# Optimization experiments

Hardware: AMD Instinct MI355X
Metric: run time of the kernel (lower is better)

The kernel has to match this reference:

```python
import jax, jax.numpy as jnp
import numpy as np

K, N, M = 65536, 4096, 64  # observations, basis centers, features


def setup_inputs() -> dict:
    key = jax.random.key(0)
    k1, k2, k3, k4 = jax.random.split(key, 4)
    x = jax.random.normal(k1, (K, M), dtype=jnp.float32)
    x_basis = jax.random.normal(k2, (N, M), dtype=jnp.float32)
    w = jax.random.normal(k3, (1, N), dtype=jnp.float32) / np.sqrt(N)
    b = jax.random.normal(k4, (1,), dtype=jnp.float32)
    return {"x": x, "x_basis": x_basis, "w": w, "b": b}


def reference(x, x_basis, w, b):
    # pairwise squared distances ||x_i - c_j||^2, [K, N]
    x2 = jnp.sum(x * x, axis=1, keepdims=True)          # [K, 1]
    c2 = jnp.sum(x_basis * x_basis, axis=1)             # [N]
    sq = x2 + c2[None, :] - 2.0 * (x @ x_basis.T)       # [K, N]
    phi = jnp.exp(-sq)                                  # gaussian RBF
    return jax.nn.sigmoid(phi @ w.T + b)                # [K, 1]
```

## Files before the change

kernel.cpp:

```cpp
#include <hip/hip_runtime.h>


#define KOBS 65536
#define NCENT 4096
#define MFEAT 64
#define BR 64
#define BN 128
#define NCHUNK (NCENT / BN)
#define KBLK (KOBS / BR)

#define SCALE_A 2.8853900817779268f
#define QS      1.4426950408889634f
#define TSKIP   -60.0f

typedef __attribute__((ext_vector_type(4)))  float float4v;
typedef __attribute__((ext_vector_type(2)))  float float2v;
typedef __attribute__((ext_vector_type(16))) float float16v;
typedef __attribute__((ext_vector_type(8)))  int   int8v;

#if __has_builtin(__builtin_amdgcn_exp2f)
#define EXP2F(x) __builtin_amdgcn_exp2f(x)
#else
#define EXP2F(x) exp2f(x)
#endif

__global__ __launch_bounds__(256) void rbf_prep(
    const float* __restrict__ xb, const float* __restrict__ w,
    char* __restrict__ cb, float2v* __restrict__ hc2w) {
    const int bid = blockIdx.x;
    const int tid = threadIdx.x;
    if (bid < 128) {
        const int o      = bid * 256 + tid;
        const int col    = o >> 3;
        const int joct   = o & 7;
        const int c      = col >> 7;
        const int w4     = (col >> 5) & 3;
        const int lanelo = col & 31;
        const int l      = lanelo + (joct >> 2) * 32;
        const int j0     = (joct & 3) * 8;
        const float* src = xb + col * MFEAT + joct * 8;
        float4v v0 = *(const float4v*)(src);
        float4v v1 = *(const float4v*)(src + 4);
        int lo = __builtin_amdgcn_cvt_pk_fp8_f32(v0[0], v0[1], 0, false);
        lo     = __builtin_amdgcn_cvt_pk_fp8_f32(v0[2], v0[3], lo, true);
        int hi = __builtin_amdgcn_cvt_pk_fp8_f32(v1[0], v1[1], 0, false);
        hi     = __builtin_amdgcn_cvt_pk_fp8_f32(v1[2], v1[3], hi, true);
        unsigned long long pk = (unsigned long long)(unsigned)lo |
                                ((unsigned long long)(unsigned)hi << 32);
        *(unsigned long long*)(cb + (size_t)((c * 4 + w4) * 64 + l) * 32 + j0) = pk;
    } else {
        const int row  = (bid - 128) * 4 + (tid >> 6);
        const int lane = tid & 63;
        float v = xb[row * MFEAT + lane];
        float s = v * v;
        #pragma unroll
        for (int off = 32; off > 0; off >>= 1) s += __shfl_xor(s, off, 64);
        if (lane == 0) {
            float2v hw = {-QS * s, w[row]};
            hc2w[row] = hw;
        }
    }
}

__global__ __launch_bounds__(256, 4) void rbf_main(
    const float* __restrict__ x, const char* __restrict__ cb,
    const float2v* __restrict__ hc2w, const float* __restrict__ bptr,
    float* __restrict__ out) {
    __shared__ float x2s[BR];
    __shared__ float zl[BR];

    const int tid  = threadIdx.x;
    const int wave = tid >> 6;
    const int lane = tid & 63;
    const int ll   = lane & 31;
    const int lh   = lane >> 5;
    const int r0   = (int)blockIdx.x * BR;

    if (tid < BR) zl[tid] = 0.0f;

    int8v af[2];
    float ssv[2];
    #pragma unroll
    for (int t = 0; t < 2; ++t) {
        const float* xr = x + (size_t)(r0 + t * 32 + ll) * MFEAT + lh * 32;
        int8v a;
        float ss = 0.0f;
        #pragma unroll
        for (int rg = 0; rg < 8; ++rg) {
            float4v v = *(const float4v*)(xr + rg * 4);
            ss = fmaf(v[0], v[0], ss); ss = fmaf(v[1], v[1], ss);
            ss = fmaf(v[2], v[2], ss); ss = fmaf(v[3], v[3], ss);
            int pk = __builtin_amdgcn_cvt_pk_fp8_f32(
                SCALE_A * v[0], SCALE_A * v[1], 0, false);
            pk = __builtin_amdgcn_cvt_pk_fp8_f32(
                SCALE_A * v[2], SCALE_A * v[3], pk, true);
            a[rg] = pk;
        }
        ss += __shfl_xor(ss, 32, 64);
        af[t]  = a;
        ssv[t] = ss;
    }
    if (wave == 0 && lh == 0) {
        x2s[ll]      = ssv[0];
        x2s[32 + ll] = ssv[1];
    }
    __syncthreads();

    const int rb = 4 * lh;
    float16v p0, p1;
    #pragma unroll
    for (int i = 0; i < 16; ++i) {
        const int ri = rb + (i & 3) + 8 * (i >> 2);
        p0[i] = -QS * x2s[ri];
        p1[i] = -QS * x2s[32 + ri];
    }

    const char* cbb = cb + wave * 2048 + lane * 32;
    const float2v* hwp = hc2w + wave * 32 + ll;

    int8v   pb[2];
    float2v phw[2];

    #define LOADB(c, s) do {                               \
        pb[s] = *(const int8v*)(cbb + (c) * 8192);         \
        float2v hw_ = hwp[(c) * 128];                      \
        hw_.x = TSKIP - hw_.x;                             \
        phw[s] = hw_;                                      \
    } while (0)

    LOADB(0, 0);

    #pragma unroll 2
    for (int c = 0; c < NCHUNK; ++c) {
        const int cur = c & 1, nxt = cur ^ 1;
        if (c + 1 < NCHUNK) LOADB(c + 1, nxt);
        __builtin_amdgcn_s_setprio(1);
        float16v a0 = __builtin_amdgcn_mfma_scale_f32_32x32x64_f8f6f4(
            af[0], pb[cur], p0, 0, 0, 0, 0x7f7f7f7f, 0, 0x7f7f7f7f);
        float16v a1 = __builtin_amdgcn_mfma_scale_f32_32x32x64_f8f6f4(
            af[1], pb[cur], p1, 0, 0, 0, 0x7f7f7f7f, 0, 0x7f7f7f7f);
        __builtin_amdgcn_s_setprio(0);
        const float tq = phw[cur].x;
        const float wv = phw[cur].y;
        #pragma unroll
        for (int t = 0; t < 2; ++t) {
            float16v av = t ? a1 : a0;
            float m0 = fmaxf(fmaxf(av[0],  av[1]),  av[2]);
            float m1 = fmaxf(fmaxf(av[3],  av[4]),  av[5]);
            float m2 = fmaxf(fmaxf(av[6],  av[7]),  av[8]);
            float m3 = fmaxf(fmaxf(av[9],  av[10]), av[11]);
            float m4 = fmaxf(fmaxf(av[12], av[13]), av[14]);
            float mx = fmaxf(fmaxf(fmaxf(m0, m1), m2),
                             fmaxf(fmaxf(m3, m4), av[15]));
            if (__any(mx > tq)) {
                const float q = TSKIP - tq;
                if (mx > tq) {
                    #pragma unroll
                    for (int i = 0; i < 16; ++i)
                        atomicAdd(&zl[t * 32 + rb + (i & 3) + 8 * (i >> 2)],
                                  wv * EXP2F(av[i] + q));
                }
            }
        }
    }

    __syncthreads();
    if (tid < BR) {
        float z = zl[tid] + bptr[0];
        out[r0 + tid] = 1.0f / (1.0f + EXP2F(-QS * z));
    }
}

extern "C" void kernel_launch(void* const* d_in, const int* in_sizes, int n_in,
                              void* d_out, int out_size, void* d_ws, size_t ws_size,
                              hipStream_t stream) {
    const float* x  = (const float*)d_in[0];
    const float* xb = (const float*)d_in[1];
    const float* w  = (const float*)d_in[2];
    const float* b  = (const float*)d_in[3];
    float* out = (float*)d_out;

    char*    cb   = (char*)d_ws;
    float2v* hc2w = (float2v*)((char*)d_ws + NCENT * MFEAT);

    rbf_prep<<<128 + NCENT / 4, 256, 0, stream>>>(xb, w, cb, hc2w);
    rbf_main<<<KBLK, 256, 0, stream>>>(x, cb, hc2w, b, out);
}
```

Before: 90.32 us.

## Fuse prep and main into one cooperative kernel using output as scratch

Replaces the separate prep and main launches with one cooperative kernel of 512 blocks by 512 threads. Grid syncs order the stages: center norms and weights are packed as bf16 metadata into the output buffer, then copied into LDS, then fp8 centers are written into the output buffer. The main loop is software-pipelined so screening of one MFMA result overlaps the next MFMA and load, and the setprio hints are dropped. This removes a launch and the workspace round trip, but adds four grid-wide barriers, bf16-rounded thresholds and weights, and reliance on the output buffer as scratch. It falls back to the old two-kernel path if the cooperative launch fails.

New measurement: 313.2 us. +246.8%, slower.

```diff
diff --git a/kernel.cpp b/kernel.cpp
--- a/kernel.cpp
+++ b/kernel.cpp
@@ -1,13 +1,13 @@
 #include <hip/hip_runtime.h>
+#include <hip/hip_cooperative_groups.h>
+
+namespace cg = cooperative_groups;
 
 
 #define KOBS 65536
 #define NCENT 4096
 #define MFEAT 64
-#define BR 64
-#define BN 128
-#define NCHUNK (NCENT / BN)
-#define KBLK (KOBS / BR)
+#define NCHUNK 32
 
 #define SCALE_A 2.8853900817779268f
 #define QS      1.4426950408889634f
@@ -17,12 +17,178 @@
 typedef __attribute__((ext_vector_type(2)))  float float2v;
 typedef __attribute__((ext_vector_type(16))) float float16v;
 typedef __attribute__((ext_vector_type(8)))  int   int8v;
+typedef __attribute__((ext_vector_type(8)))  short short8;
 
 #if __has_builtin(__builtin_amdgcn_exp2f)
 #define EXP2F(x) __builtin_amdgcn_exp2f(x)
 #else
 #define EXP2F(x) exp2f(x)
 #endif
+
+static __device__ inline unsigned short f2bfu(float f) {
+    unsigned int u = __float_as_uint(f);
+    return (unsigned short)((u + 0x7fffu + ((u >> 16) & 1u)) >> 16);
+}
+
+#define MFMA(A, B, C) __builtin_amdgcn_mfma_scale_f32_32x32x64_f8f6f4( \
+    (A), (B), (C), 0, 0, 0, 0x7f7f7f7f, 0, 0x7f7f7f7f)
+
+__global__ __launch_bounds__(512, 4) void rbf_fused(
+    const float* __restrict__ x, const float* __restrict__ xb,
+    const float* __restrict__ w, const float* __restrict__ bptr,
+    float* __restrict__ out) {
+    __shared__ unsigned int meta_s[NCENT];
+    __shared__ float x2s[128];
+    __shared__ float zl[128];
+
+    const int tid  = threadIdx.x;
+    const int wv   = tid >> 6;
+    const int lane = tid & 63;
+    const int ll   = lane & 31;
+    const int lh   = lane >> 5;
+    const int rt   = wv >> 2;
+    const int wq   = wv & 3;
+    const int bid  = (int)blockIdx.x;
+
+    cg::grid_group grid = cg::this_grid();
+
+    const int n = bid * 8 + wv;
+    const float cv = xb[n * MFEAT + lane];
+    {
+        float s = cv * cv;
+        #pragma unroll
+        for (int off = 32; off > 0; off >>= 1) s += __shfl_xor(s, off, 64);
+        if (lane == 0) {
+            const float tq = TSKIP + QS * s;
+            ((unsigned int*)out)[n] =
+                ((unsigned int)f2bfu(tq) << 16) | f2bfu(w[n]);
+        }
+    }
+
+    const int r0e = bid * 128 + rt * 64;
+    int8v af0, af1;
+    #pragma unroll
+    for (int t = 0; t < 2; ++t) {
+        const float* xr = x + (size_t)(r0e + t * 32 + ll) * MFEAT + lh * 32;
+        int8v a;
+        float ss = 0.0f;
+        #pragma unroll
+        for (int rg = 0; rg < 8; ++rg) {
+            float4v v = *(const float4v*)(xr + rg * 4);
+            ss = fmaf(v[0], v[0], ss); ss = fmaf(v[1], v[1], ss);
+            ss = fmaf(v[2], v[2], ss); ss = fmaf(v[3], v[3], ss);
+            int pk = __builtin_amdgcn_cvt_pk_fp8_f32(
+                SCALE_A * v[0], SCALE_A * v[1], 0, false);
+            pk = __builtin_amdgcn_cvt_pk_fp8_f32(
+                SCALE_A * v[2], SCALE_A * v[3], pk, true);
+            a[rg] = pk;
+        }
+        ss += __shfl_xor(ss, 32, 64);
+        if (t == 0) af0 = a; else af1 = a;
+        if (wq == 0 && lh == 0) x2s[rt * 64 + t * 32 + ll] = ss;
+    }
+    if (tid < 128) zl[tid] = 0.0f;
+
+    grid.sync();
+
+    {
+        const unsigned int* mo = (const unsigned int*)out;
+        #pragma unroll
+        for (int i = 0; i < NCENT / 512; ++i) meta_s[tid + i * 512] = mo[tid + i * 512];
+    }
+
+    grid.sync();
+
+    {
+        const unsigned int u8 =
+            (unsigned int)__builtin_amdgcn_cvt_pk_fp8_f32(cv, cv, 0, false) & 0xffu;
+        const int cc  = n >> 7;
+        const int wc  = (n >> 5) & 3;
+        const int llc = n & 31;
+        ((unsigned char*)out)[(size_t)((cc * 4 + wc) * 64 + llc + (lane >> 5) * 32) * 32
+                              + (lane & 31)] = (unsigned char)u8;
+    }
+
+    const int rb = 4 * lh;
+    float16v p0, p1;
+    #pragma unroll
+    for (int i = 0; i < 16; ++i) {
+        const int ri = rb + (i & 3) + 8 * (i >> 2);
+        p0[i] = -QS * x2s[rt * 64 + ri];
+        p1[i] = -QS * x2s[rt * 64 + 32 + ri];
+    }
+
+    grid.sync();
+
+    const int zbase = rt * 64 + rb;
+    const int moff  = wq * 32 + ll;
+    const char* cbb = (const char*)out + (size_t)(wq * 64 + lane) * 32;
+
+    #define SCREEN(AV, TQ, WV, TOFF) do {                                     \
+        float m0_ = fmaxf(fmaxf((AV)[0],  (AV)[1]),  (AV)[2]);                \
+        float m1_ = fmaxf(fmaxf((AV)[3],  (AV)[4]),  (AV)[5]);                \
+        float m2_ = fmaxf(fmaxf((AV)[6],  (AV)[7]),  (AV)[8]);                \
+        float m3_ = fmaxf(fmaxf((AV)[9],  (AV)[10]), (AV)[11]);               \
+        float m4_ = fmaxf(fmaxf((AV)[12], (AV)[13]), (AV)[14]);               \
+        float mx_ = fmaxf(fmaxf(fmaxf(m0_, m1_), m2_),                        \
+                          fmaxf(fmaxf(m3_, m4_), (AV)[15]));                  \
+        if (__any(mx_ > (TQ))) {                                              \
+            if (mx_ > (TQ)) {                                                 \
+                const float q_ = TSKIP - (TQ);                                \
+                _Pragma("unroll")                                             \
+                for (int i_ = 0; i_ < 16; ++i_)                               \
+                    atomicAdd(&zl[zbase + (TOFF) + (i_ & 3) + 8 * (i_ >> 2)], \
+                              (WV) * EXP2F((AV)[i_] + q_));                   \
+            }                                                                 \
+        }                                                                     \
+    } while (0)
+
+    int8v pbE = *(const int8v*)(cbb);
+    int8v pbO = *(const int8v*)(cbb + 8192);
+    unsigned int mu0 = meta_s[moff];
+    float tq_p = __uint_as_float(mu0 & 0xffff0000u);
+    float w_p  = __uint_as_float(mu0 << 16);
+    float16v avA = MFMA(af0, pbE, p0);
+    float16v avB = MFMA(af1, pbE, p1);
+    pbE = *(const int8v*)(cbb + 2 * 8192);
+    SCREEN(avA, tq_p, w_p, 0);
+
+    #define BODY(C, PB, DOLOAD) do {                                          \
+        const unsigned int mu_ = meta_s[(C) * 128 + moff];                    \
+        const float tq_c = __uint_as_float(mu_ & 0xffff0000u);                \
+        const float w_c  = __uint_as_float(mu_ << 16);                        \
+        float16v nA = MFMA(af0, PB, p0);                                      \
+        SCREEN(avB, tq_p, w_p, 32);                             \
+        float16v nB = MFMA(af1, PB, p1);                                      \
+        if (DOLOAD) PB = *(const int8v*)(cbb + (size_t)((C) + 2) * 8192);     \
+        SCREEN(nA, tq_c, w_c, 0);                                \
+        avB = nB; tq_p = tq_c; w_p = w_c;                                     \
+    } while (0)
+
+    for (int c2 = 1; c2 < 31; c2 += 2) {
+        BODY(c2,     pbO, (c2 + 2 <= 31));
+        BODY(c2 + 1, pbE, (c2 + 3 <= 31));
+    }
+    {
+        const unsigned int mu_ = meta_s[31 * 128 + moff];
+        const float tq_c = __uint_as_float(mu_ & 0xffff0000u);
+        const float w_c  = __uint_as_float(mu_ << 16);
+        float16v nA = MFMA(af0, pbO, p0);
+        SCREEN(avB, tq_p, w_p, 32);
+        float16v nB = MFMA(af1, pbO, p1);
+        SCREEN(nA, tq_c, w_c, 0);
+        SCREEN(nB, tq_c, w_c, 32);
+    }
+    #undef BODY
+    #undef SCREEN
+
+    grid.sync();
+
+    if (tid < 128) {
+        const float z = zl[tid] + bptr[0];
+        out[bid * 128 + tid] = 1.0f / (1.0f + EXP2F(-QS * z));
+    }
+}
 
 __global__ __launch_bounds__(256) void rbf_prep(
     const float* __restrict__ xb, const float* __restrict__ w,
@@ -66,17 +232,17 @@
     const float* __restrict__ x, const char* __restrict__ cb,
     const float2v* __restrict__ hc2w, const float* __restrict__ bptr,
     float* __restrict__ out) {
-    __shared__ float x2s[BR];
-    __shared__ float zl[BR];
+    __shared__ float x2s[64];
+    __shared__ float zl[64];
 
     const int tid  = threadIdx.x;
     const int wave = tid >> 6;
     const int lane = tid & 63;
     const int ll   = lane & 31;
     const int lh   = lane >> 5;
-    const int r0   = (int)blockIdx.x * BR;
-
-    if (tid < BR) zl[tid] = 0.0f;
+    const int r0   = (int)blockIdx.x * 64;
+
+    if (tid < 64) zl[tid] = 0.0f;
 
     int8v af[2];
     float ssv[2];
@@ -134,14 +300,10 @@
     for (int c = 0; c < NCHUNK; ++c) {
         const int cur = c & 1, nxt = cur ^ 1;
         if (c + 1 < NCHUNK) LOADB(c + 1, nxt);
-        __builtin_amdgcn_s_setprio(1);
-        float16v a0 = __builtin_amdgcn_mfma_scale_f32_32x32x64_f8f6f4(
-            af[0], pb[cur], p0, 0, 0, 0, 0x7f7f7f7f, 0, 0x7f7f7f7f);
-        float16v a1 = __builtin_amdgcn_mfma_scale_f32_32x32x64_f8f6f4(
-            af[1], pb[cur], p1, 0, 0, 0, 0x7f7f7f7f, 0, 0x7f7f7f7f);
-        __builtin_amdgcn_s_setprio(0);
+        float16v a0 = MFMA(af[0], pb[cur], p0);
+        float16v a1 = MFMA(af[1], pb[cur], p1);
         const float tq = phw[cur].x;
-        const float wv = phw[cur].y;
+        const float wvv = phw[cur].y;
         #pragma unroll
         for (int t = 0; t < 2; ++t) {
             float16v av = t ? a1 : a0;
@@ -153,19 +315,20 @@
             float mx = fmaxf(fmaxf(fmaxf(m0, m1), m2),
                              fmaxf(fmaxf(m3, m4), av[15]));
             if (__any(mx > tq)) {
-                const float q = TSKIP - tq;
                 if (mx > tq) {
+                    const float q = TSKIP - tq;
                     #pragma unroll
                     for (int i = 0; i < 16; ++i)
                         atomicAdd(&zl[t * 32 + rb + (i & 3) + 8 * (i >> 2)],
-                                  wv * EXP2F(av[i] + q));
+                                  wvv * EXP2F(av[i] + q));
                 }
             }
         }
     }
+    #undef LOADB
 
     __syncthreads();
-    if (tid < BR) {
+    if (tid < 64) {
         float z = zl[tid] + bptr[0];
         out[r0 + tid] = 1.0f / (1.0f + EXP2F(-QS * z));
     }
@@ -180,9 +343,14 @@
     const float* b  = (const float*)d_in[3];
     float* out = (float*)d_out;
 
-    char*    cb   = (char*)d_ws;
-    float2v* hc2w = (float2v*)((char*)d_ws + NCENT * MFEAT);
-
-    rbf_prep<<<128 + NCENT / 4, 256, 0, stream>>>(xb, w, cb, hc2w);
-    rbf_main<<<KBLK, 256, 0, stream>>>(x, cb, hc2w, b, out);
-}
+    void* kargs[5] = {(void*)&x, (void*)&xb, (void*)&w, (void*)&b, (void*)&out};
+    hipError_t err = hipLaunchCooperativeKernel(
+        (const void*)rbf_fused, dim3(512), dim3(512), kargs, 0, stream);
+    if (err != hipSuccess) {
+        (void)hipGetLastError();
+        char*    cb   = (char*)d_ws;
+        float2v* hc2w = (float2v*)((char*)d_ws + NCENT * MFEAT);
+        rbf_prep<<<128 + NCENT / 4, 256, 0, stream>>>(xb, w, cb, hc2w);
+        rbf_main<<<KOBS / 64, 256, 0, stream>>>(x, cb, hc2w, b, out);
+    }
+}
```
